# Performance work log

Hardware: AMD Instinct MI355X
Metric: run time of the kernel (lower is better)

The kernel has to match this reference:

```python
import jax, jax.numpy as jnp
import numpy as np

B, T, N, K, IB, O = 128, 16, 65536, 8, 256, 10

def setup_inputs() -> dict:
    key = jax.random.key(0)
    ks = jax.random.split(key, 8)
    x = jax.random.randint(ks[0], (B, T, IB), 0, 2, dtype=jnp.int32)          # boolean input bits per timestep
    adj_list = jax.random.randint(ks[1], (N, K), 0, N, dtype=jnp.int32)       # incoming neighbors, homogenized
    adj_mask = jnp.ones((N, K), dtype=jnp.int32)                               # validity mask (all valid here)
    lut = jax.random.randint(ks[2], (N, 2 ** K), 0, 2, dtype=jnp.int32)        # boolean lookup table per node
    init_state = jax.random.randint(ks[3], (N,), 0, 2, dtype=jnp.int32)        # 'random' init strategy
    w_in = jnp.arange(IB, dtype=jnp.int32)                                     # input-bit -> node index map
    w_readout = jax.random.normal(ks[4], (O, N), dtype=jnp.float32) * 0.01
    b_readout = jax.random.normal(ks[5], (O,), dtype=jnp.float32)
    return dict(x=x, adj_list=adj_list, adj_mask=adj_mask, lut=lut,
                init_state=init_state, w_in=w_in,
                w_readout=w_readout, b_readout=b_readout)

def _run_reservoir(x, adj_list, adj_mask, lut, init_state, w_in):
    # x: [B,T,IB] bits; returns final boolean state [B,N] (int32)
    powers = (2 ** jnp.arange(K, dtype=jnp.int32))[::-1]   # matches powers_of_2 flip
    node_idx = jnp.arange(N, dtype=jnp.int32)
    state0 = jnp.broadcast_to(init_state[None, :], (B, N)).astype(jnp.int32)

    def step(state, xt):
        # perturb input nodes with this timestep's bits (xor perturbation)
        state = state.at[:, w_in].set(jnp.bitwise_xor(state[:, w_in], xt))
        # gather incoming-neighbor states, mask padded slots: [B,N,K]
        neigh = jnp.take(state, adj_list, axis=1) * adj_mask
        # pack K bits into LUT index, MSB-first: [B,N]
        idx = jnp.sum(neigh * powers, axis=-1)
        # per-node boolean update via LUT gather
        new_state = lut[node_idx[None, :], idx]
        return new_state, None

    xT = jnp.swapaxes(x, 0, 1)  # [T,B,IB]
    final, _ = jax.lax.scan(step, state0, xT)
    return final

def reference(x, adj_list, adj_mask, lut, init_state, w_in, w_readout, b_readout):
    final = _run_reservoir(x, adj_list, adj_mask, lut, init_state, w_in)
    logits = final.astype(jnp.float32) @ w_readout.T + b_readout  # [B,O]
    return jax.nn.sigmoid(logits)
```

## Files before the change

kernel.cpp:

```cpp
#include <hip/hip_runtime.h>
#include <stdint.h>

#define NN     65536
#define KK     8
#define BB     128
#define TT     16
#define IBITS  256
#define OO     10

#define ZIDX         (NN + IBITS)
#define SBUF_ENTRIES (NN + IBITS + 1)
#define RCHUNKS 512
#define RNODES  128

#if defined(__has_builtin)
#  if __has_builtin(__builtin_amdgcn_sbfe)
#    define HAVE_SBFE 1
#  endif
#endif

__device__ __forceinline__ uint32_t bmask(uint32_t w, int off) {
#ifdef HAVE_SBFE
  return (uint32_t)__builtin_amdgcn_sbfe((int)w, off, 1);
#else
  return 0u - ((w >> off) & 1u);
#endif
}

__device__ __forceinline__ uint4 xorv(uint4 a, uint4 b) {
  return make_uint4(a.x ^ b.x, a.y ^ b.y, a.z ^ b.z, a.w ^ b.w);
}

template<int D, int BASE> struct Anf1 {
  static __device__ __forceinline__ uint32_t eval(const uint32_t (&L)[8],
                                                  const uint32_t (&xv)[8],
                                                  uint32_t x01) {
    uint32_t lo = Anf1<D - 1, BASE>::eval(L, xv, x01);
    uint32_t hi = Anf1<D - 1, BASE + (1 << (D - 1))>::eval(L, xv, x01);
    return lo ^ (xv[D - 1] & hi);
  }
};
template<int BASE> struct Anf1<2, BASE> {
  static __device__ __forceinline__ uint32_t eval(const uint32_t (&L)[8],
                                                  const uint32_t (&xv)[8],
                                                  uint32_t x01) {
    const uint32_t lw = L[BASE >> 5];
    const uint32_t c0 = bmask(lw, (BASE & 31) + 0);
    const uint32_t c1 = bmask(lw, (BASE & 31) + 1);
    const uint32_t c2 = bmask(lw, (BASE & 31) + 2);
    const uint32_t c3 = bmask(lw, (BASE & 31) + 3);
    return c0 ^ (xv[0] & c1) ^ (xv[1] & c2) ^ (x01 & c3);
  }
};

__global__ __launch_bounds__(256) void pack_lut_kernel(const int* __restrict__ lut,
                                                       uint32_t* __restrict__ lutanf) {
  const int g = blockIdx.x * 256 + threadIdx.x;
  const int n = g >> 3, w = g & 7;
  const int4* lut4 = (const int4*)lut;
  uint32_t val = 0;
#pragma unroll
  for (int q = 0; q < 8; ++q) {
    int4 v = lut4[n * 64 + w * 8 + q];
    val |= (uint32_t)(v.x & 1) << (4 * q + 0);
    val |= (uint32_t)(v.y & 1) << (4 * q + 1);
    val |= (uint32_t)(v.z & 1) << (4 * q + 2);
    val |= (uint32_t)(v.w & 1) << (4 * q + 3);
  }
  val ^= (val << 1)  & 0xAAAAAAAAu;
  val ^= (val << 2)  & 0xCCCCCCCCu;
  val ^= (val << 4)  & 0xF0F0F0F0u;
  val ^= (val << 8)  & 0xFF00FF00u;
  val ^= (val << 16) & 0xFFFF0000u;
  uint32_t p;
  p = __shfl_xor(val, 1, 64); val ^= p & (0u - (uint32_t)(w & 1));
  p = __shfl_xor(val, 2, 64); val ^= p & (0u - (uint32_t)((w >> 1) & 1));
  p = __shfl_xor(val, 4, 64); val ^= p & (0u - (uint32_t)((w >> 2) & 1));
  lutanf[g] = val;
}

__global__ __launch_bounds__(256) void pack_madj_kernel(const int* __restrict__ adj,
                                                        const int* __restrict__ adjm,
                                                        int* __restrict__ madj) {
  const int g = blockIdx.x * 256 + threadIdx.x;
  int a = adj[g];
  int m = adjm[g] & 1;
  madj[g] = m ? ((a < IBITS) ? a + NN : a) : ZIDX;
}

__global__ __launch_bounds__(256) void pack_x_kernel(const int* __restrict__ x,
                                                     uint32_t* __restrict__ xvecw) {
  const int g = blockIdx.x * 256 + threadIdx.x;
  const int t = g >> 10, rest = g & 1023, i = rest >> 2, bq = rest & 3;
  uint32_t wv = 0;
#pragma unroll
  for (int bl = 0; bl < 32; ++bl) {
    int b = bq * 32 + bl;
    uint32_t bit = (uint32_t)(x[(b * TT + t) * IBITS + i] & 1);
    wv |= bit << bl;
  }
  xvecw[(t * IBITS + i) * 4 + bq] = wv;
}

__global__ __launch_bounds__(256) void pack_state_kernel(const int* __restrict__ init,
                                                         const uint4* __restrict__ xvec0,
                                                         uint4* __restrict__ sA,
                                                         uint4* __restrict__ sB) {
  const int n = blockIdx.x * 256 + threadIdx.x;
  uint32_t m = 0u - (uint32_t)(init[n] & 1);
  uint4 s = make_uint4(m, m, m, m);
  sA[n] = s;
  if (n < IBITS) sA[NN + n] = xorv(s, xvec0[n]);
  if (n == 0) {
    uint4 z = make_uint4(0, 0, 0, 0);
    sA[ZIDX] = z;
    sB[ZIDX] = z;
  }
}

__global__ __launch_bounds__(256) void step_kernel(const uint32_t* __restrict__ sinw,
                                                   uint32_t* __restrict__ soutw,
                                                   const uint4* __restrict__ lutanf,
                                                   const int* __restrict__ madj,
                                                   const uint32_t* __restrict__ xnextw) {
  const int g = blockIdx.x * 256 + threadIdx.x;
  const int n = g >> 2, w = g & 3;
  const int4* madj4 = (const int4*)madj;
  int4 a0 = madj4[n * 2 + 0], a1 = madj4[n * 2 + 1];
  uint4 l0 = lutanf[n * 2 + 0], l1 = lutanf[n * 2 + 1];
  const int ia[8] = {a0.x, a0.y, a0.z, a0.w, a1.x, a1.y, a1.z, a1.w};
  uint32_t xv[8];
#pragma unroll
  for (int k = 0; k < 8; ++k) {
    xv[7 - k] = sinw[(ia[k] << 2) + w];
  }
  const uint32_t L[8] = {l0.x, l0.y, l0.z, l0.w, l1.x, l1.y, l1.z, l1.w};
  const uint32_t x01 = xv[0] & xv[1];
  uint32_t r = Anf1<8, 0>::eval(L, xv, x01);
  soutw[(n << 2) + w] = r;
  if (xnextw != nullptr && n < IBITS) {
    soutw[((NN + n) << 2) + w] = r ^ xnextw[(n << 2) + w];
  }
}

__global__ __launch_bounds__(256) void readout_kernel(const uint32_t* __restrict__ statew,
                                                      const float* __restrict__ w,
                                                      float* __restrict__ part) {
  __shared__ uint32_t sw[64 * 4];
  __shared__ float wsm[OO * 64];
  const int c = blockIdx.x;
  const int t = threadIdx.x;
  const int b = t & 127, oh = t >> 7;
  const int word = b >> 5, sh = b & 31;
  float acc[5] = {0.f, 0.f, 0.f, 0.f, 0.f};
  for (int s = 0; s < 2; ++s) {
    const int base = c * RNODES + s * 64;
    __syncthreads();
    sw[t] = statew[base * 4 + t];
#pragma unroll
    for (int r = 0; r < 3; ++r) {
      int idx = r * 256 + t;
      if (idx < OO * 64) wsm[idx] = w[(idx >> 6) * NN + base + (idx & 63)];
    }
    __syncthreads();
#pragma unroll 8
    for (int j = 0; j < 64; ++j) {
      uint32_t m = 0u - ((sw[j * 4 + word] >> sh) & 1u);
#pragma unroll
      for (int q = 0; q < 5; ++q) {
        uint32_t wv = __float_as_uint(wsm[(oh * 5 + q) * 64 + j]) & m;
        acc[q] += __uint_as_float(wv);
      }
    }
  }
#pragma unroll
  for (int q = 0; q < 5; ++q)
    part[(c * BB + b) * OO + oh * 5 + q] = acc[q];
}

__global__ __launch_bounds__(256) void finalize_kernel(const float* __restrict__ part,
                                                       const float* __restrict__ bias,
                                                       float* __restrict__ out) {
  __shared__ float red[256];
  const int i = blockIdx.x;
  const int b = i / OO, o = i % OO;
  const int t = threadIdx.x;
  float s = part[(t * BB + b) * OO + o] + part[((t + 256) * BB + b) * OO + o];
  red[t] = s;
  __syncthreads();
  for (int h = 128; h > 0; h >>= 1) {
    if (t < h) red[t] += red[t + h];
    __syncthreads();
  }
  if (t == 0) out[b * OO + o] = 1.f / (1.f + __expf(-(red[0] + bias[o])));
}

extern "C" void kernel_launch(void* const* d_in, const int* in_sizes, int n_in,
                              void* d_out, int out_size, void* d_ws, size_t ws_size,
                              hipStream_t stream) {
  const int* x    = (const int*)d_in[0];
  const int* adj  = (const int*)d_in[1];
  const int* adjm = (const int*)d_in[2];
  const int* lut  = (const int*)d_in[3];
  const int* init = (const int*)d_in[4];
  const float* wro = (const float*)d_in[6];
  const float* bro = (const float*)d_in[7];
  float* out = (float*)d_out;

  char* ws = (char*)d_ws;
  const size_t SBUF = (size_t)SBUF_ENTRIES * 16;
  uint4* sA       = (uint4*)(ws);
  uint4* sB       = (uint4*)(ws + SBUF);
  uint32_t* xvecw = (uint32_t*)(ws + 2 * SBUF);
  uint32_t* lutanf = (uint32_t*)(ws + 2 * SBUF + (size_t)TT * IBITS * 16);
  int* madj       = (int*)(ws + 2 * SBUF + (size_t)TT * IBITS * 16 + (size_t)NN * 32);
  float* part     = (float*)(ws + 2 * SBUF + (size_t)TT * IBITS * 16 + (size_t)NN * 64);

  hipLaunchKernelGGL(pack_lut_kernel, dim3((NN * KK) / 256), dim3(256), 0, stream, lut, lutanf);
  hipLaunchKernelGGL(pack_x_kernel, dim3((TT * IBITS * 4) / 256), dim3(256), 0, stream, x, xvecw);
  hipLaunchKernelGGL(pack_madj_kernel, dim3((NN * KK) / 256), dim3(256), 0, stream, adj, adjm, madj);
  hipLaunchKernelGGL(pack_state_kernel, dim3(NN / 256), dim3(256), 0, stream,
                     init, (const uint4*)xvecw, sA, sB);

  for (int t = 0; t < TT; ++t) {
    const uint32_t* sin = (const uint32_t*)((t & 1) ? sB : sA);
    uint32_t* sout      = (uint32_t*)((t & 1) ? sA : sB);
    const uint32_t* xn  = (t + 1 < TT) ? (xvecw + (size_t)(t + 1) * IBITS * 4) : nullptr;
    hipLaunchKernelGGL(step_kernel, dim3((NN * 4) / 256), dim3(256), 0, stream,
                       sin, sout, (const uint4*)lutanf, madj, xn);
  }
  hipLaunchKernelGGL(readout_kernel, dim3(RCHUNKS), dim3(256), 0, stream,
                     (const uint32_t*)sA, wro, part);
  hipLaunchKernelGGL(finalize_kernel, dim3(BB * OO), dim3(256), 0, stream, part, bro, out);
}
```

Measured before the change: 271.8 us.

## Replace ANF evaluation with mux tree, fuse prep kernels, two words per thread

Stops converting the LUT to algebraic normal form and evaluates it directly as a bitsliced Shannon mux tree on the raw truth table. Each thread now handles two of the four batch words with uint2 loads, which halves the thread count and shares the LUT and adjacency loads between two evaluations. The four prep kernels are merged into one launch, and the first timestep's input bits are computed inline. The mux tree spends about three ops per node against two for the ANF form, and the change also trades parallelism for per-thread reuse.

```diff
diff --git a/kernel.cpp b/kernel.cpp
--- a/kernel.cpp
+++ b/kernel.cpp
@@ -13,133 +13,128 @@
 #define RCHUNKS 512
 #define RNODES  128
 
-#if defined(__has_builtin)
-#  if __has_builtin(__builtin_amdgcn_sbfe)
-#    define HAVE_SBFE 1
-#  endif
-#endif
-
 __device__ __forceinline__ uint32_t bmask(uint32_t w, int off) {
-#ifdef HAVE_SBFE
   return (uint32_t)__builtin_amdgcn_sbfe((int)w, off, 1);
-#else
-  return 0u - ((w >> off) & 1u);
-#endif
-}
-
-__device__ __forceinline__ uint4 xorv(uint4 a, uint4 b) {
-  return make_uint4(a.x ^ b.x, a.y ^ b.y, a.z ^ b.z, a.w ^ b.w);
-}
-
-template<int D, int BASE> struct Anf1 {
-  static __device__ __forceinline__ uint32_t eval(const uint32_t (&L)[8],
-                                                  const uint32_t (&xv)[8],
-                                                  uint32_t x01) {
-    uint32_t lo = Anf1<D - 1, BASE>::eval(L, xv, x01);
-    uint32_t hi = Anf1<D - 1, BASE + (1 << (D - 1))>::eval(L, xv, x01);
-    return lo ^ (xv[D - 1] & hi);
+}
+__device__ __forceinline__ uint32_t mux(uint32_t s, uint32_t hi, uint32_t lo) {
+  return ((hi ^ lo) & s) ^ lo;
+}
+
+template<int D, int BASE> struct Sh {
+  static __device__ __forceinline__ void eval(const uint32_t (&L)[8],
+      const uint32_t (&xa)[8], const uint32_t (&xb)[8],
+      uint32_t &ra, uint32_t &rb) {
+    uint32_t la, lb, ha, hb;
+    Sh<D - 1, BASE>::eval(L, xa, xb, la, lb);
+    Sh<D - 1, BASE + (1 << (D - 1))>::eval(L, xa, xb, ha, hb);
+    ra = mux(xa[D - 1], ha, la);
+    rb = mux(xb[D - 1], hb, lb);
   }
 };
-template<int BASE> struct Anf1<2, BASE> {
-  static __device__ __forceinline__ uint32_t eval(const uint32_t (&L)[8],
-                                                  const uint32_t (&xv)[8],
-                                                  uint32_t x01) {
+template<int BASE> struct Sh<2, BASE> {
+  static __device__ __forceinline__ void eval(const uint32_t (&L)[8],
+      const uint32_t (&xa)[8], const uint32_t (&xb)[8],
+      uint32_t &ra, uint32_t &rb) {
     const uint32_t lw = L[BASE >> 5];
     const uint32_t c0 = bmask(lw, (BASE & 31) + 0);
     const uint32_t c1 = bmask(lw, (BASE & 31) + 1);
     const uint32_t c2 = bmask(lw, (BASE & 31) + 2);
     const uint32_t c3 = bmask(lw, (BASE & 31) + 3);
-    return c0 ^ (xv[0] & c1) ^ (xv[1] & c2) ^ (x01 & c3);
+    uint32_t t0, t1;
+    t0 = mux(xa[0], c1, c0); t1 = mux(xa[0], c3, c2); ra = mux(xa[1], t1, t0);
+    t0 = mux(xb[0], c1, c0); t1 = mux(xb[0], c3, c2); rb = mux(xb[1], t1, t0);
   }
 };
 
-__global__ __launch_bounds__(256) void pack_lut_kernel(const int* __restrict__ lut,
-                                                       uint32_t* __restrict__ lutanf) {
-  const int g = blockIdx.x * 256 + threadIdx.x;
-  const int n = g >> 3, w = g & 7;
-  const int4* lut4 = (const int4*)lut;
-  uint32_t val = 0;
-#pragma unroll
-  for (int q = 0; q < 8; ++q) {
-    int4 v = lut4[n * 64 + w * 8 + q];
-    val |= (uint32_t)(v.x & 1) << (4 * q + 0);
-    val |= (uint32_t)(v.y & 1) << (4 * q + 1);
-    val |= (uint32_t)(v.z & 1) << (4 * q + 2);
-    val |= (uint32_t)(v.w & 1) << (4 * q + 3);
-  }
-  val ^= (val << 1)  & 0xAAAAAAAAu;
-  val ^= (val << 2)  & 0xCCCCCCCCu;
-  val ^= (val << 4)  & 0xF0F0F0F0u;
-  val ^= (val << 8)  & 0xFF00FF00u;
-  val ^= (val << 16) & 0xFFFF0000u;
-  uint32_t p;
-  p = __shfl_xor(val, 1, 64); val ^= p & (0u - (uint32_t)(w & 1));
-  p = __shfl_xor(val, 2, 64); val ^= p & (0u - (uint32_t)((w >> 1) & 1));
-  p = __shfl_xor(val, 4, 64); val ^= p & (0u - (uint32_t)((w >> 2) & 1));
-  lutanf[g] = val;
-}
-
-__global__ __launch_bounds__(256) void pack_madj_kernel(const int* __restrict__ adj,
-                                                        const int* __restrict__ adjm,
-                                                        int* __restrict__ madj) {
-  const int g = blockIdx.x * 256 + threadIdx.x;
-  int a = adj[g];
-  int m = adjm[g] & 1;
-  madj[g] = m ? ((a < IBITS) ? a + NN : a) : ZIDX;
-}
-
-__global__ __launch_bounds__(256) void pack_x_kernel(const int* __restrict__ x,
-                                                     uint32_t* __restrict__ xvecw) {
-  const int g = blockIdx.x * 256 + threadIdx.x;
-  const int t = g >> 10, rest = g & 1023, i = rest >> 2, bq = rest & 3;
-  uint32_t wv = 0;
-#pragma unroll
-  for (int bl = 0; bl < 32; ++bl) {
-    int b = bq * 32 + bl;
-    uint32_t bit = (uint32_t)(x[(b * TT + t) * IBITS + i] & 1);
-    wv |= bit << bl;
-  }
-  xvecw[(t * IBITS + i) * 4 + bq] = wv;
-}
-
-__global__ __launch_bounds__(256) void pack_state_kernel(const int* __restrict__ init,
-                                                         const uint4* __restrict__ xvec0,
-                                                         uint4* __restrict__ sA,
-                                                         uint4* __restrict__ sB) {
-  const int n = blockIdx.x * 256 + threadIdx.x;
-  uint32_t m = 0u - (uint32_t)(init[n] & 1);
-  uint4 s = make_uint4(m, m, m, m);
-  sA[n] = s;
-  if (n < IBITS) sA[NN + n] = xorv(s, xvec0[n]);
-  if (n == 0) {
-    uint4 z = make_uint4(0, 0, 0, 0);
-    sA[ZIDX] = z;
-    sB[ZIDX] = z;
+#define PB_LUT   2048
+#define PB_MADJ  2048
+#define PB_X     64
+#define PB_STATE 256
+#define PREP_BLOCKS (PB_LUT + PB_MADJ + PB_X + PB_STATE)
+
+__global__ __launch_bounds__(256) void prep_kernel(
+    const int* __restrict__ lut, const int* __restrict__ adj,
+    const int* __restrict__ adjm, const int* __restrict__ x,
+    const int* __restrict__ init,
+    uint32_t* __restrict__ luttt, int* __restrict__ madj,
+    uint32_t* __restrict__ xvecw, uint4* __restrict__ sA, uint4* __restrict__ sB) {
+  const int b = blockIdx.x, t = threadIdx.x;
+  if (b < PB_LUT) {
+    const int g = b * 256 + t;
+    const int n = g >> 3, w = g & 7;
+    const int4* lut4 = (const int4*)lut;
+    uint32_t val = 0;
+#pragma unroll
+    for (int q = 0; q < 8; ++q) {
+      int4 v = lut4[n * 64 + w * 8 + q];
+      val |= (uint32_t)(v.x & 1) << (4 * q + 0);
+      val |= (uint32_t)(v.y & 1) << (4 * q + 1);
+      val |= (uint32_t)(v.z & 1) << (4 * q + 2);
+      val |= (uint32_t)(v.w & 1) << (4 * q + 3);
+    }
+    luttt[g] = val;
+  } else if (b < PB_LUT + PB_MADJ) {
+    const int g = (b - PB_LUT) * 256 + t;
+    int a = adj[g];
+    int m = adjm[g] & 1;
+    madj[g] = m ? ((a < IBITS) ? a + NN : a) : ZIDX;
+  } else if (b < PB_LUT + PB_MADJ + PB_X) {
+    const int g = (b - PB_LUT - PB_MADJ) * 256 + t;
+    const int tt = g >> 10, rest = g & 1023, i = rest >> 2, bq = rest & 3;
+    uint32_t wv = 0;
+#pragma unroll
+    for (int bl = 0; bl < 32; ++bl) {
+      int bb = bq * 32 + bl;
+      wv |= (uint32_t)(x[(bb * TT + tt) * IBITS + i] & 1) << bl;
+    }
+    xvecw[(tt * IBITS + i) * 4 + bq] = wv;
+  } else {
+    const int n = (b - PB_LUT - PB_MADJ - PB_X) * 256 + t;
+    uint32_t m = 0u - (uint32_t)(init[n] & 1);
+    uint4 s = make_uint4(m, m, m, m);
+    sA[n] = s;
+    if (n < IBITS) {
+      uint32_t wv[4] = {0, 0, 0, 0};
+#pragma unroll
+      for (int bb = 0; bb < BB; ++bb) {
+        uint32_t bit = (uint32_t)(x[(bb * TT + 0) * IBITS + n] & 1);
+        wv[bb >> 5] |= bit << (bb & 31);
+      }
+      sA[NN + n] = make_uint4(s.x ^ wv[0], s.y ^ wv[1], s.z ^ wv[2], s.w ^ wv[3]);
+    }
+    if (n == 0) {
+      uint4 z = make_uint4(0, 0, 0, 0);
+      sA[ZIDX] = z;
+      sB[ZIDX] = z;
+    }
   }
 }
 
 __global__ __launch_bounds__(256) void step_kernel(const uint32_t* __restrict__ sinw,
                                                    uint32_t* __restrict__ soutw,
-                                                   const uint4* __restrict__ lutanf,
+                                                   const uint4* __restrict__ luttt,
                                                    const int* __restrict__ madj,
                                                    const uint32_t* __restrict__ xnextw) {
   const int g = blockIdx.x * 256 + threadIdx.x;
-  const int n = g >> 2, w = g & 3;
+  const int n = g >> 1, h = g & 1;
   const int4* madj4 = (const int4*)madj;
   int4 a0 = madj4[n * 2 + 0], a1 = madj4[n * 2 + 1];
-  uint4 l0 = lutanf[n * 2 + 0], l1 = lutanf[n * 2 + 1];
+  uint4 l0 = luttt[n * 2 + 0], l1 = luttt[n * 2 + 1];
   const int ia[8] = {a0.x, a0.y, a0.z, a0.w, a1.x, a1.y, a1.z, a1.w};
-  uint32_t xv[8];
+  uint32_t xa[8], xb[8];
 #pragma unroll
   for (int k = 0; k < 8; ++k) {
-    xv[7 - k] = sinw[(ia[k] << 2) + w];
+    uint2 gg = *(const uint2*)(sinw + (ia[k] << 2) + (h << 1));
+    xa[7 - k] = gg.x;
+    xb[7 - k] = gg.y;
   }
   const uint32_t L[8] = {l0.x, l0.y, l0.z, l0.w, l1.x, l1.y, l1.z, l1.w};
-  const uint32_t x01 = xv[0] & xv[1];
-  uint32_t r = Anf1<8, 0>::eval(L, xv, x01);
-  soutw[(n << 2) + w] = r;
+  uint32_t ra, rb;
+  Sh<8, 0>::eval(L, xa, xb, ra, rb);
+  *(uint2*)(soutw + (n << 2) + (h << 1)) = make_uint2(ra, rb);
   if (xnextw != nullptr && n < IBITS) {
-    soutw[((NN + n) << 2) + w] = r ^ xnextw[(n << 2) + w];
+    uint2 xn = *(const uint2*)(xnextw + (n << 2) + (h << 1));
+    *(uint2*)(soutw + ((NN + n) << 2) + (h << 1)) = make_uint2(ra ^ xn.x, rb ^ xn.y);
   }
 }
 
@@ -209,25 +204,22 @@
 
   char* ws = (char*)d_ws;
   const size_t SBUF = (size_t)SBUF_ENTRIES * 16;
-  uint4* sA       = (uint4*)(ws);
-  uint4* sB       = (uint4*)(ws + SBUF);
-  uint32_t* xvecw = (uint32_t*)(ws + 2 * SBUF);
-  uint32_t* lutanf = (uint32_t*)(ws + 2 * SBUF + (size_t)TT * IBITS * 16);
-  int* madj       = (int*)(ws + 2 * SBUF + (size_t)TT * IBITS * 16 + (size_t)NN * 32);
-  float* part     = (float*)(ws + 2 * SBUF + (size_t)TT * IBITS * 16 + (size_t)NN * 64);
-
-  hipLaunchKernelGGL(pack_lut_kernel, dim3((NN * KK) / 256), dim3(256), 0, stream, lut, lutanf);
-  hipLaunchKernelGGL(pack_x_kernel, dim3((TT * IBITS * 4) / 256), dim3(256), 0, stream, x, xvecw);
-  hipLaunchKernelGGL(pack_madj_kernel, dim3((NN * KK) / 256), dim3(256), 0, stream, adj, adjm, madj);
-  hipLaunchKernelGGL(pack_state_kernel, dim3(NN / 256), dim3(256), 0, stream,
-                     init, (const uint4*)xvecw, sA, sB);
+  uint4* sA        = (uint4*)(ws);
+  uint4* sB        = (uint4*)(ws + SBUF);
+  uint32_t* xvecw  = (uint32_t*)(ws + 2 * SBUF);
+  uint32_t* luttt  = (uint32_t*)(ws + 2 * SBUF + (size_t)TT * IBITS * 16);
+  int* madj        = (int*)(ws + 2 * SBUF + (size_t)TT * IBITS * 16 + (size_t)NN * 32);
+  float* part      = (float*)(ws + 2 * SBUF + (size_t)TT * IBITS * 16 + (size_t)NN * 64);
+
+  hipLaunchKernelGGL(prep_kernel, dim3(PREP_BLOCKS), dim3(256), 0, stream,
+                     lut, adj, adjm, x, init, luttt, madj, xvecw, sA, sB);
 
   for (int t = 0; t < TT; ++t) {
     const uint32_t* sin = (const uint32_t*)((t & 1) ? sB : sA);
     uint32_t* sout      = (uint32_t*)((t & 1) ? sA : sB);
     const uint32_t* xn  = (t + 1 < TT) ? (xvecw + (size_t)(t + 1) * IBITS * 4) : nullptr;
-    hipLaunchKernelGGL(step_kernel, dim3((NN * 4) / 256), dim3(256), 0, stream,
-                       sin, sout, (const uint4*)lutanf, madj, xn);
+    hipLaunchKernelGGL(step_kernel, dim3((NN * 2) / 256), dim3(256), 0, stream,
+                       sin, sout, (const uint4*)luttt, madj, xn);
   }
   hipLaunchKernelGGL(readout_kernel, dim3(RCHUNKS), dim3(256), 0, stream,
                      (const uint32_t*)sA, wro, part);
```

After: 296.0 us. 1.09x slower.
